# Performance work log

Hardware: AMD Instinct MI355X
Metric: run time of the kernel (lower is better)

## Reference

```python
import jax, jax.numpy as jnp
import numpy as np

B, T, N, F = 8, 24, 207, 16
H = 64            # hidden_dim
DH = 16           # dims_hyper[-1] / node-embedding out
DA = 4 * F        # temporal attention dim_out
DS = 64           # ss_gal gcn out dim (last_ss_gal_dim)
GDEP = 2
ALPHA, BETA, GAMMA = 0.05, 0.95, 0.95
TA = 2.0


def _lin(x, w, b=None):
    y = x @ w
    return y if b is None else y + b


def gcn_hyper(x, A, W, b):
    # x: [B,N,C], A: [N,N] static. h <- a*x + g * einsum('nvc,vw->nwc', h, A)
    h = x
    outs = [h]
    for _ in range(GDEP):
        h = ALPHA * x + GAMMA * jnp.einsum('bvc,vw->bwc', h, A)
        outs.append(h)
    return _lin(jnp.concatenate(outs, axis=-1), W, b)


def gcn_gru(x, A_dyn, A_sta, W, b):
    # x: [B,N,C], A_dyn: [B,N,N], A_sta: [N,N]
    h = x
    outs = [h]
    for _ in range(GDEP):
        h = (ALPHA * x
             + BETA * jnp.einsum('bvw,bvc->bwc', A_dyn, h)     # bmm(A^T, h)
             + GAMMA * jnp.einsum('bvc,vw->bwc', h, A_sta))
        outs.append(h)
    return _lin(jnp.concatenate(outs, axis=-1), W, b)


def gcn_ssgal(x, A, W, b):
    # x: [B*,N,C], A: [B*,N,N]
    h = x
    outs = [h]
    for _ in range(GDEP):
        h = ALPHA * x + GAMMA * jnp.einsum('bvw,bvc->bwc', A, h)
        outs.append(h)
    return _lin(jnp.concatenate(outs, axis=-1), W, b)


def setup_inputs() -> dict:
    key = jax.random.key(0)
    ks = jax.random.split(key, 32)
    i = iter(range(32))
    w = lambda *s: (0.02 * jax.random.normal(ks[next(i)], s, dtype=jnp.float32))
    inp = {
        'input_sequence': jax.random.normal(ks[next(i)], (B, T, N, F), dtype=jnp.float32),
        'static_adj': jax.random.uniform(ks[next(i)], (N, N), dtype=jnp.float32),
        # hyper graph generators: mlp in = (GDEP+1)*H -> DH
        'src_gen_w': w((GDEP + 1) * H, DH), 'src_gen_b': w(DH),
        'tgt_gen_w': w((GDEP + 1) * H, DH), 'tgt_gen_b': w(DH),
        # node embeddings: F -> DH
        'src_emb_w': w(F, DH), 'src_emb_b': w(DH),
        'tgt_emb_w': w(F, DH), 'tgt_emb_b': w(DH),
        # GRU gate GCNs: mlp in = (GDEP+1)*(F+H) -> H
        'gru_z_w': w((GDEP + 1) * (F + H), H), 'gru_z_b': w(H),
        'gru_r_w': w((GDEP + 1) * (F + H), H), 'gru_r_b': w(H),
        'gru_c_w': w((GDEP + 1) * (F + H), H), 'gru_c_b': w(H),
        # temporal attention: F -> DA, score DA -> 1
        'attn_q_w': w(F, DA),
        'attn_k_w': w(F, DA), 'attn_k_b': w(DA),
        'attn_s_w': w(DA, 1),
        # ss_gal spatial gcn: (GDEP+1)*F -> DS
        'sgcn_w': w((GDEP + 1) * F, DS), 'sgcn_b': w(DS),
        # predictors
        'short_w': w(DS, F), 'short_b': w(F),
        'long_w': w(H, F), 'long_b': w(F),
        'fus_w': w(DS + H, F), 'fus_b': w(F),
    }
    return inp


def _forward(input_sequence, static_adj,
             src_gen_w, src_gen_b, tgt_gen_w, tgt_gen_b,
             src_emb_w, src_emb_b, tgt_emb_w, tgt_emb_b,
             gru_z_w, gru_z_b, gru_r_w, gru_r_b, gru_c_w, gru_c_b,
             attn_q_w, attn_k_w, attn_k_b, attn_s_w,
             sgcn_w, sgcn_b,
             short_w, short_b, long_w, long_b, fus_w, fus_b):
    batch, steps, nodes = input_sequence.shape[0], input_sequence.shape[1], input_sequence.shape[2]
    eye = jnp.eye(nodes, dtype=input_sequence.dtype)

    def cell(x_t, h):
        # x_t: [B,N,F], h: [B,N,H]
        src_ctx = gcn_hyper(h, static_adj, src_gen_w, src_gen_b)   # [B,N,DH]
        tgt_ctx = gcn_hyper(h, static_adj, tgt_gen_w, tgt_gen_b)
        s = jnp.tanh(TA * _lin(x_t, src_emb_w, src_emb_b) * src_ctx)
        t = jnp.tanh(TA * _lin(x_t, tgt_emb_w, tgt_emb_b) * tgt_ctx)
        asym = jnp.einsum('bnc,bmc->bnm', s, t) - jnp.einsum('bnc,bmc->bnm', t, s)
        adj = jax.nn.relu(jnp.tanh(TA * asym)) + eye
        adj = adj / (adj.sum(axis=-1, keepdims=True) + 1e-8)
        gi = jnp.concatenate([x_t, h], axis=-1)
        z = jax.nn.sigmoid(gcn_gru(gi, adj, static_adj, gru_z_w, gru_z_b))
        r = jax.nn.sigmoid(gcn_gru(gi, adj, static_adj, gru_r_w, gru_r_b))
        ri = jnp.concatenate([x_t, r * h], axis=-1)
        c = jnp.tanh(gcn_gru(ri, adj, static_adj, gru_c_w, gru_c_b))
        return z * h + (1.0 - z) * c

    h = jnp.zeros((batch, nodes, H), dtype=input_sequence.dtype)
    for t_step in range(0, max(1, steps - 4), 4):
        h = cell(input_sequence[:, t_step], h)

    # ss_gal branch on the last 4 steps
    recent = input_sequence[:, -4:]            # [B,4,N,F]
    target = input_sequence[:, -1]             # [B,N,F]
    # temporal attention
    q = target @ attn_q_w                      # [B,N,DA]
    k = recent @ attn_k_w + attn_k_b           # [B,4,N,DA]
    scores = jnp.tanh(q[:, None, :, None, :] + k[:, :, None, :, :])  # [B,4,N,N,DA]
    scores = jnp.squeeze(scores @ attn_s_w, axis=-1)                  # [B,4,N,N]
    attn = jax.nn.softmax(scores, axis=-1)
    dyn_adj = static_adj[None] + attn.reshape(-1, nodes, nodes)       # [B*4,N,N]
    rh = recent.reshape(-1, nodes, recent.shape[-1])                  # [B*4,N,F]
    rh = gcn_ssgal(rh, dyn_adj, sgcn_w, sgcn_b)                       # [B*4,N,DS]
    rh = jax.nn.relu(rh.reshape(batch, -1, nodes, rh.shape[-1]))      # [B,4,N,DS]
    target = jnp.sum(rh, axis=1)                                       # [B,N,DS]

    short = _lin(target, short_w, short_b)      # [B,N,F]
    h = cell(short, h)                          # final GRU step on short-term prediction
    long = _lin(h, long_w, long_b)              # [B,N,F]
    fused = _lin(jnp.concatenate([target, h], axis=-1), fus_w, fus_b)  # [B,N,F]
    return jnp.stack([short, long, fused], axis=0)  # [3,B,N,F]


def reference(input_sequence, static_adj,
              src_gen_w, src_gen_b, tgt_gen_w, tgt_gen_b,
              src_emb_w, src_emb_b, tgt_emb_w, tgt_emb_b,
              gru_z_w, gru_z_b, gru_r_w, gru_r_b, gru_c_w, gru_c_b,
              attn_q_w, attn_k_w, attn_k_b, attn_s_w,
              sgcn_w, sgcn_b,
              short_w, short_b, long_w, long_b, fus_w, fus_b):
    return _forward(input_sequence, static_adj,
                    src_gen_w, src_gen_b, tgt_gen_w, tgt_gen_b,
                    src_emb_w, src_emb_b, tgt_emb_w, tgt_emb_b,
                    gru_z_w, gru_z_b, gru_r_w, gru_r_b, gru_c_w, gru_c_b,
                    attn_q_w, attn_k_w, attn_k_b, attn_s_w,
                    sgcn_w, sgcn_b,
                    short_w, short_b, long_w, long_b, fus_w, fus_b)
```

## Files before the change

kernel.cpp:

```cpp
#include <hip/hip_runtime.h>


constexpr int B = 8, T = 24, N = 207, F = 16, H = 64, DH = 16;
constexpr int PS = 208;
constexpr float ALPHA = 0.05f, BETA = 0.95f, GAMMA = 0.95f, TA = 2.0f;
constexpr int NF = N * F;
constexpr int BNF = B * N * F;

__device__ __forceinline__ float tanh_fast(float x) { float e = __expf(2.f * x); return 1.f - 2.f / (e + 1.f); }
__device__ __forceinline__ float sigm(float x) { return 1.f / (1.f + __expf(-x)); }
__device__ __forceinline__ float tanh_pnc(float x) {
    float x2 = x * x;
    float p = x * (27.f + x2);
    float q = 27.f + 9.f * x2;
    return p * __builtin_amdgcn_rcpf(q);
}

__global__ __launch_bounds__(256) void k_build_Ts(const float* __restrict__ adj, float* __restrict__ Ts) {
    int i = blockIdx.x * 256 + threadIdx.x;
    if (i >= N * N) return;
    int w = i / N, v = i % N;
    Ts[(size_t)w * PS + v] = adj[v * N + w];
}

__global__ __launch_bounds__(256) void k_mm_sq(const float* __restrict__ Ain, float* __restrict__ Aout) {
    const float* A = Ain;
    float* O = Aout;
    int w0 = blockIdx.x * 32, v0b = blockIdx.y * 32;
    int tid = threadIdx.x;
    __shared__ float sA[2][32][33], sB[2][32][33];
    float acc[4] = {0, 0, 0, 0};
    int i0 = tid >> 5, j = tid & 31;
    int r = tid >> 3, c4 = (tid & 7) * 4;
    float4 av, bv;
    auto loadT = [&](int u0) {
        av = make_float4(0, 0, 0, 0); bv = make_float4(0, 0, 0, 0);
        int w = w0 + r, u = u0 + r;
        if (w < N) av = *(const float4*)&A[(size_t)w * PS + u0 + c4];
        if (u < N) bv = *(const float4*)&A[(size_t)u * PS + v0b + c4];
    };
    loadT(0);
    int cur = 0;
    for (int t = 0; t < 7; t++) {
        __syncthreads();
        sA[cur][r][c4] = av.x; sA[cur][r][c4 + 1] = av.y; sA[cur][r][c4 + 2] = av.z; sA[cur][r][c4 + 3] = av.w;
        sB[cur][r][c4] = bv.x; sB[cur][r][c4 + 1] = bv.y; sB[cur][r][c4 + 2] = bv.z; sB[cur][r][c4 + 3] = bv.w;
        if (t < 6) loadT((t + 1) * 32);
        __syncthreads();
#pragma unroll 8
        for (int u_ = 0; u_ < 32; u_++) {
            float bvv = sB[cur][u_][j];
#pragma unroll
            for (int k = 0; k < 4; k++) acc[k] += sA[cur][i0 + k * 8][u_] * bvv;
        }
        cur ^= 1;
    }
#pragma unroll
    for (int k = 0; k < 4; k++) {
        int w = w0 + i0 + k * 8, v = v0b + j;
        if (w < N && v < N) O[(size_t)w * PS + v] = acc[k];
    }
}

__global__ __launch_bounds__(256) void k_cell_a(
    const float* __restrict__ h, const float* __restrict__ Ts, const float* __restrict__ A2,
    const float* __restrict__ xseq, int tsel, const float* __restrict__ xbuf,
    const float* __restrict__ Wsrc, const float* __restrict__ bsrc,
    const float* __restrict__ Wtgt, const float* __restrict__ btgt,
    const float* __restrict__ Wes, const float* __restrict__ bes,
    const float* __restrict__ Wet, const float* __restrict__ bet,
    float* __restrict__ s_out, float* __restrict__ t_out, float* __restrict__ catg) {
    int b = blockIdx.y, w0 = blockIdx.x * 16, lane = blockIdx.z;
    int tid = threadIdx.x, ty = tid >> 4, tx = tid & 15;
    __shared__ float sTs[2][16][33], sA2[2][16][33];
    __shared__ float sH[2][32][64];
    __shared__ float cat[16][193];
    __shared__ float sW[192][16];
    __shared__ float sX[16][16], sWe[16][16];
    float au[4] = {0, 0, 0, 0}, aw[4] = {0, 0, 0, 0};
    const float* hb = h + b * N * H;
    const float* xp = (tsel >= 0) ? (xseq + ((size_t)(b * T + tsel)) * NF) : (xbuf + (size_t)b * NF);
    int pidx = tid & 127;
    int pr = pidx >> 3, pc4 = (pidx & 7) * 4;
    float4 t4;
    float4 h4[2];
    int hr[2], hc[2];
#pragma unroll
    for (int k = 0; k < 2; k++) { int l4 = tid + k * 256; hr[k] = l4 >> 4; hc[k] = (l4 & 15) * 4; }
    auto loadT = [&](int v0) {
        t4 = make_float4(0, 0, 0, 0);
        const float* src = (tid < 128) ? Ts : A2;
        int w = w0 + pr;
        if (w < N) t4 = *(const float4*)&src[(size_t)w * PS + v0 + pc4];
#pragma unroll
        for (int k = 0; k < 2; k++) {
            float4 hv = make_float4(0, 0, 0, 0);
            int v = v0 + hr[k];
            if (v < N) hv = *(const float4*)&hb[(size_t)v * H + hc[k]];
            h4[k] = hv;
        }
    };
    loadT(0);
    int cur = 0;
    for (int t = 0; t < 7; t++) {
        __syncthreads();
        {
            float (*dst)[33] = (tid < 128) ? sTs[cur] : sA2[cur];
            dst[pr][pc4] = t4.x; dst[pr][pc4 + 1] = t4.y; dst[pr][pc4 + 2] = t4.z; dst[pr][pc4 + 3] = t4.w;
        }
#pragma unroll
        for (int k = 0; k < 2; k++) *(float4*)&sH[cur][hr[k]][hc[k]] = h4[k];
        if (t < 6) loadT((t + 1) * 32);
        __syncthreads();
#pragma unroll 8
        for (int v = 0; v < 32; v++) {
            float pu = sTs[cur][ty][v], pw = sA2[cur][ty][v];
#pragma unroll
            for (int j = 0; j < 4; j++) {
                float x = sH[cur][v][tx * 4 + j];
                au[j] += pu * x; aw[j] += pw * x;
            }
        }
        cur ^= 1;
    }
    int w = w0 + ty;
    bool valid = w < N;
    __syncthreads();
    if (valid) {
#pragma unroll
        for (int j = 0; j < 4; j++) {
            int c = tx * 4 + j;
            float hv = hb[(size_t)w * H + c];
            float u = au[j], w2 = aw[j];
            cat[ty][c] = hv;
            cat[ty][64 + c] = ALPHA * hv + GAMMA * u;
            cat[ty][128 + c] = ALPHA * hv + ALPHA * GAMMA * u + GAMMA * GAMMA * w2;
        }
    } else {
#pragma unroll
        for (int j = 0; j < 4; j++) {
            int c = tx * 4 + j;
            cat[ty][c] = 0; cat[ty][64 + c] = 0; cat[ty][128 + c] = 0;
        }
    }
    const float* Wg = lane ? Wtgt : Wsrc;
    const float* bg = lane ? btgt : bsrc;
    const float* We = lane ? Wet : Wes;
    const float* be = lane ? bet : bes;
    {
        float4 wv[3];
#pragma unroll
        for (int k = 0; k < 3; k++) wv[k] = *(const float4*)&Wg[(tid + k * 256) * 4];
        float4 xv = make_float4(0, 0, 0, 0), ev = make_float4(0, 0, 0, 0);
        int sr = 0, sc = 0;
        if (tid < 64) {
            sr = tid >> 2; sc = (tid & 3) * 4;
            int n = w0 + sr;
            if (n < N) xv = *(const float4*)&xp[(size_t)n * F + sc];
            ev = *(const float4*)&We[tid * 4];
        }
#pragma unroll
        for (int k = 0; k < 3; k++) {
            int l4 = tid + k * 256;
            int r = l4 >> 2, c4 = (l4 & 3) * 4;
            *(float4*)&sW[r][c4] = wv[k];
        }
        if (tid < 64) {
            *(float4*)&sX[sr][sc] = xv;
            *(float4*)&sWe[sr][sc] = ev;
        }
    }
    __syncthreads();
    if (lane == 0 && valid) {
#pragma unroll
        for (int j = 0; j < 5; j++) {
            int c = tx * 5 + j;
            float v = (c < 16) ? sX[ty][c] : hb[(size_t)w * H + (c - 16)];
            catg[((size_t)(b * N + w)) * 240 + c] = v;
        }
    }
    {
        float ctx = bg[tx];
#pragma unroll 8
        for (int c = 0; c < 192; c++) ctx += cat[ty][c] * sW[c][tx];
        float xe = be[tx];
#pragma unroll
        for (int f = 0; f < 16; f++) xe += sX[ty][f] * sWe[f][tx];
        if (valid) {
            float val = tanh_fast(TA * xe * ctx);
            if (lane == 0) s_out[(size_t)(b * N + w) * DH + tx] = val;
            else           t_out[(size_t)(b * N + w) * DH + tx] = val;
        }
    }
}

__global__ __launch_bounds__(256) void k_cell_bP(const float* __restrict__ s_in, const float* __restrict__ t_in,
                                                 const float* __restrict__ adj, float* __restrict__ P) {
    int b = blockIdx.y, v0 = blockIdx.x * 16;
    int tid = threadIdx.x, ty = tid >> 4, tx = tid & 15;
    __shared__ float sS[N][17], sT[N][17];
    for (int l4 = tid; l4 < 828; l4 += 256) {
        float4 sv = *(const float4*)&s_in[(size_t)b * N * 16 + l4 * 4];
        float4 tv = *(const float4*)&t_in[(size_t)b * N * 16 + l4 * 4];
        int r = l4 >> 2, c = (l4 & 3) * 4;
        sS[r][c] = sv.x; sS[r][c + 1] = sv.y; sS[r][c + 2] = sv.z; sS[r][c + 3] = sv.w;
        sT[r][c] = tv.x; sT[r][c + 1] = tv.y; sT[r][c + 2] = tv.z; sT[r][c + 3] = tv.w;
    }
    __syncthreads();
    int v = v0 + ty;
    bool valid = v < N;
    int vc = valid ? v : (N - 1);
    float sv[16], tv[16];
#pragma unroll
    for (int k = 0; k < 16; k++) { sv[k] = sS[vc][k]; tv[k] = sT[vc][k]; }
    float val[13];
    float rsum = 0.f;
#pragma unroll
    for (int idx = 0; idx < 13; idx++) {
        int w = tx + 16 * idx;
        float r = 0.f;
        if (w < N) {
            float a = 0.f;
#pragma unroll
            for (int k = 0; k < 16; k++) a += sv[k] * sT[w][k] - tv[k] * sS[w][k];
            r = tanh_fast(TA * a);
            r = r > 0.f ? r : 0.f;
            if (w == v) r += 1.f;
        }
        val[idx] = r;
        rsum += r;
    }
    float tot = rsum;
    for (int d = 8; d > 0; d >>= 1) tot += __shfl_down(tot, d, 16);
    tot = __shfl(tot, 0, 16);
    float rinv = BETA / (tot + 1e-8f);
    if (valid) {
        float* Pb = P + (size_t)b * PS * PS;
#pragma unroll
        for (int idx = 0; idx < 13; idx++) {
            int w = tx + 16 * idx;
            if (w < N) Pb[(size_t)w * PS + v] = val[idx] * rinv + GAMMA * adj[v * N + w];
        }
    }
}

__global__ __launch_bounds__(256) void k_prop1(const float* __restrict__ P, float* __restrict__ cat) {
    int b = blockIdx.y, w0 = blockIdx.x * 16, c0 = blockIdx.z * 16;
    int tid = threadIdx.x, ty = tid >> 4, tx = tid & 15;
    const float* Pb = P + (size_t)b * PS * PS;
    __shared__ float sP[2][16][33], sX[2][32][17];
    float a1 = 0.f;
    int pr = tid >> 4, pc = (tid & 15) * 2;
    int xr = tid >> 3, xc = (tid & 7) * 2;
    float2 pv, xv;
    auto loadT = [&](int v0) {
        pv = make_float2(0, 0); xv = make_float2(0, 0);
        int w = w0 + pr;
        if (w < N) pv = *(const float2*)&Pb[(size_t)w * PS + v0 + pc];
        int vv = v0 + xr;
        if (vv < N) xv = *(const float2*)&cat[((size_t)(b * N + vv)) * 240 + c0 + xc];
    };
    loadT(0);
    int cur = 0;
    for (int t = 0; t < 7; t++) {
        __syncthreads();
        sP[cur][pr][pc] = pv.x; sP[cur][pr][pc + 1] = pv.y;
        sX[cur][xr][xc] = xv.x; sX[cur][xr][xc + 1] = xv.y;
        if (t < 6) loadT((t + 1) * 32);
        __syncthreads();
#pragma unroll 8
        for (int v_ = 0; v_ < 32; v_++) a1 += sP[cur][ty][v_] * sX[cur][v_][tx];
        cur ^= 1;
    }
    int w = w0 + ty, c = c0 + tx;
    if (w < N) {
        size_t base = ((size_t)(b * N + w)) * 240;
        cat[base + 80 + c] = ALPHA * cat[base + c] + a1;
    }
}

__global__ __launch_bounds__(256) void k_gate(
    const float* __restrict__ cat, const float* __restrict__ P,
    const float* __restrict__ Wa, const float* __restrict__ ba,
    const float* __restrict__ Wb, const float* __restrict__ bb,
    int baseMode,
    const float* __restrict__ xseq, int tsel, const float* __restrict__ xbuf,
    float* __restrict__ zbuf, float* __restrict__ ricat,
    float* __restrict__ h,
    const float* __restrict__ target,
    const float* __restrict__ Wlong, const float* __restrict__ blong,
    const float* __restrict__ Wfus, const float* __restrict__ bfus,
    float* __restrict__ out) {
    int mode = baseMode + blockIdx.z;
    const float* W = (mode == 1) ? Wb : Wa;
    const float* bias = (mode == 1) ? bb : ba;
    int b = blockIdx.y, w0 = blockIdx.x * 16;
    int tid = threadIdx.x, ty = tid >> 4, tx = tid & 15;
    const float* Pb = P + (size_t)b * PS * PS;
    __shared__ float sC[16][241];
    __shared__ float sP[16][33];
    __shared__ float sX[32][81];
    __shared__ float sW[48][65];
    __shared__ float hrow[16][65], trow[16][65];
    for (int l4 = tid; l4 < 640; l4 += 256) {
        int r = l4 / 40, c4 = (l4 % 40) * 4;
        int w = w0 + r;
        float4 v4 = make_float4(0, 0, 0, 0);
        if (w < N) v4 = *(const float4*)&cat[((size_t)(b * N + w)) * 240 + c4];
        sC[r][c4] = v4.x; sC[r][c4 + 1] = v4.y; sC[r][c4 + 2] = v4.z; sC[r][c4 + 3] = v4.w;
    }
    float acc[5] = {0, 0, 0, 0, 0};
    int prr = tid >> 4, prc = (tid & 15) * 2;
    int xrow = tid & 31, xc0 = (tid >> 5) * 10;
    float2 pv;
    float2 xv[5];
    auto loadT = [&](int v0) {
        pv = make_float2(0, 0);
        int w = w0 + prr;
        if (w < N) pv = *(const float2*)&Pb[(size_t)w * PS + v0 + prc];
        int v = v0 + xrow;
#pragma unroll
        for (int k = 0; k < 5; k++) xv[k] = make_float2(0, 0);
        if (v < N) {
            const float* src = &cat[((size_t)(b * N + v)) * 240 + 80 + xc0];
#pragma unroll
            for (int k = 0; k < 5; k++) xv[k] = *(const float2*)&src[k * 2];
        }
    };
    loadT(0);
    for (int t = 0; t < 7; t++) {
        __syncthreads();
        sP[prr][prc] = pv.x; sP[prr][prc + 1] = pv.y;
#pragma unroll
        for (int k = 0; k < 5; k++) { sX[xrow][xc0 + 2 * k] = xv[k].x; sX[xrow][xc0 + 2 * k + 1] = xv[k].y; }
        if (t < 6) loadT((t + 1) * 32);
        __syncthreads();
#pragma unroll 8
        for (int v = 0; v < 32; v++) {
            float p = sP[ty][v];
#pragma unroll
            for (int j = 0; j < 5; j++) acc[j] += p * sX[v][tx * 5 + j];
        }
    }
#pragma unroll
    for (int j = 0; j < 5; j++) {
        int c = tx * 5 + j;
        sC[ty][160 + c] = ALPHA * sC[ty][c] + acc[j];
    }
    float4 wv[3];
#pragma unroll
    for (int k = 0; k < 3; k++) wv[k] = *(const float4*)&W[(tid + k * 256) * 4];
    float ga[4];
#pragma unroll
    for (int j = 0; j < 4; j++) ga[j] = bias[tx * 4 + j];
    for (int ch = 0; ch < 5; ch++) {
        __syncthreads();
#pragma unroll
        for (int k = 0; k < 3; k++) {
            int l4 = tid + k * 256;
            int r = l4 >> 4, cc = (l4 & 15) * 4;
            sW[r][cc] = wv[k].x; sW[r][cc + 1] = wv[k].y; sW[r][cc + 2] = wv[k].z; sW[r][cc + 3] = wv[k].w;
        }
        if (ch < 4) {
#pragma unroll
            for (int k = 0; k < 3; k++) wv[k] = *(const float4*)&W[(size_t)(ch + 1) * 3072 + (tid + k * 256) * 4];
        }
        __syncthreads();
        int c0 = ch * 48;
#pragma unroll 8
        for (int cc = 0; cc < 48; cc++) {
            float cv = sC[ty][c0 + cc];
#pragma unroll
            for (int j = 0; j < 4; j++) ga[j] += cv * sW[cc][tx * 4 + j];
        }
    }
    int w = w0 + ty;
    bool valid = w < N;
    if (mode == 0) {
        if (valid) {
#pragma unroll
            for (int j = 0; j < 4; j++) zbuf[((size_t)(b * N + w)) * 64 + tx * 4 + j] = sigm(ga[j]);
        }
    } else if (mode == 1) {
        if (valid) {
#pragma unroll
            for (int j = 0; j < 4; j++) {
                int o = tx * 4 + j;
                ricat[((size_t)(b * N + w)) * 240 + 16 + o] = sigm(ga[j]) * h[((size_t)(b * N + w)) * 64 + o];
            }
            if (tx < 4) {
                const float* xp = (tsel >= 0) ? (xseq + ((size_t)(b * T + tsel)) * NF) : (xbuf + (size_t)b * NF);
#pragma unroll
                for (int j = 0; j < 4; j++) {
                    int c = tx * 4 + j;
                    ricat[((size_t)(b * N + w)) * 240 + c] = xp[w * F + c];
                }
            }
        }
    } else {
#pragma unroll
        for (int j = 0; j < 4; j++) {
            int o = tx * 4 + j;
            float cval = tanh_fast(ga[j]);
            float zv = 0.f, hv = 0.f;
            if (valid) { zv = zbuf[((size_t)(b * N + w)) * 64 + o]; hv = h[((size_t)(b * N + w)) * 64 + o]; }
            float hn = zv * hv + (1.f - zv) * cval;
            if (valid) h[((size_t)(b * N + w)) * 64 + o] = hn;
            hrow[ty][o] = valid ? hn : 0.f;
        }
        if (mode == 3) {
            for (int l = tid; l < 1024; l += 256) {
                int i = l >> 6, o = l & 63;
                int ww = w0 + i;
                trow[i][o] = (ww < N) ? target[((size_t)(b * N + ww)) * 64 + o] : 0.f;
            }
            __syncthreads();
            float lg = blong[tx];
            float fs = bfus[tx];
            for (int o = 0; o < 64; o++) {
                lg += hrow[ty][o] * Wlong[o * 16 + tx];
                fs += trow[ty][o] * Wfus[o * 16 + tx] + hrow[ty][o] * Wfus[(64 + o) * 16 + tx];
            }
            if (valid) {
                out[((size_t)1 * B * N + b * N + w) * 16 + tx] = lg;
                out[((size_t)2 * B * N + b * N + w) * 16 + tx] = fs;
            }
        }
    }
}

__global__ __launch_bounds__(256) void k_attn2(const float* __restrict__ inp,
                                               const float* __restrict__ Wq, const float* __restrict__ Wk,
                                               const float* __restrict__ kb, const float* __restrict__ sw_,
                                               float* __restrict__ attnT, float* __restrict__ rsum) {
    int bt = blockIdx.z, b = bt >> 2, tau = bt & 3;
    int n0 = blockIdx.x * 32, m0 = blockIdx.y * 32;
    int tid = threadIdx.x, ti = tid >> 4, tj = tid & 15;
    __shared__ float sQ[32][65], sK[32][65];
    __shared__ float sWq[16][64], sWk[16][64];
    __shared__ float sXq[32][17], sXk[32][17];
    __shared__ float ssw[64], skb[64];
    const float* xq = inp + ((size_t)(b * T + (T - 1))) * NF;
    const float* xk = inp + ((size_t)(b * T + 20 + tau)) * NF;
    {
        float4 wq4 = *(const float4*)&Wq[tid * 4];
        float4 wk4 = *(const float4*)&Wk[tid * 4];
        *(float4*)&sWq[tid >> 4][(tid & 15) * 4] = wq4;
        *(float4*)&sWk[tid >> 4][(tid & 15) * 4] = wk4;
        if (tid < 64) { ssw[tid] = sw_[tid]; skb[tid] = kb[tid]; }
        int idx = tid & 127;
        int r = idx >> 2, c4 = (idx & 3) * 4;
        if (tid < 128) {
            float4 a = make_float4(0, 0, 0, 0);
            int n = n0 + r;
            if (n < N) a = *(const float4*)&xq[(size_t)n * F + c4];
            sXq[r][c4] = a.x; sXq[r][c4 + 1] = a.y; sXq[r][c4 + 2] = a.z; sXq[r][c4 + 3] = a.w;
        } else {
            float4 c = make_float4(0, 0, 0, 0);
            int m = m0 + r;
            if (m < N) c = *(const float4*)&xk[(size_t)m * F + c4];
            sXk[r][c4] = c.x; sXk[r][c4 + 1] = c.y; sXk[r][c4 + 2] = c.z; sXk[r][c4 + 3] = c.w;
        }
    }
    __syncthreads();
    {
        int r = tid >> 3, o0 = (tid & 7) * 8;
        float xr[16], xkr[16];
#pragma unroll
        for (int f = 0; f < 16; f++) { xr[f] = sXq[r][f]; xkr[f] = sXk[r][f]; }
#pragma unroll
        for (int j = 0; j < 8; j++) {
            int o = o0 + j;
            float aq = 0.f, ak = skb[o];
#pragma unroll
            for (int f = 0; f < 16; f++) { aq += xr[f] * sWq[f][o]; ak += xkr[f] * sWk[f][o]; }
            sQ[r][o] = aq; sK[r][o] = ak;
        }
    }
    __syncthreads();
    float s00 = 0.f, s01 = 0.f, s10 = 0.f, s11 = 0.f;
#pragma unroll 2
    for (int d = 0; d < 64; d++) {
        float w = ssw[d];
        float q1 = sQ[ti][d], q2 = sQ[ti + 16][d];
        float k1 = sK[tj][d], k2 = sK[tj + 16][d];
        s00 += tanh_pnc(q1 + k1) * w;
        s01 += tanh_pnc(q1 + k2) * w;
        s10 += tanh_pnc(q2 + k1) * w;
        s11 += tanh_pnc(q2 + k2) * w;
    }
    int n1 = n0 + ti, n2 = n0 + ti + 16, m1 = m0 + tj, m2 = m0 + tj + 16;
    bool vn1 = n1 < N, vn2 = n2 < N, vm1 = m1 < N, vm2 = m2 < N;
    float e00 = (vn1 && vm1) ? __expf(s00) : 0.f;
    float e01 = (vn1 && vm2) ? __expf(s01) : 0.f;
    float e10 = (vn2 && vm1) ? __expf(s10) : 0.f;
    float e11 = (vn2 && vm2) ? __expf(s11) : 0.f;
    float part1 = e00 + e01, part2 = e10 + e11;
    for (int d = 8; d > 0; d >>= 1) {
        part1 += __shfl_down(part1, d, 16);
        part2 += __shfl_down(part2, d, 16);
    }
    if (tj == 0) {
        if (vn1) atomicAdd(&rsum[bt * N + n1], part1);
        if (vn2) atomicAdd(&rsum[bt * N + n2], part2);
    }
    __syncthreads();
    float* tile = &sQ[0][0];
    tile[tj * 33 + ti] = e00;
    tile[(tj + 16) * 33 + ti] = e01;
    tile[tj * 33 + ti + 16] = e10;
    tile[(tj + 16) * 33 + ti + 16] = e11;
    __syncthreads();
    {
        int row = tid >> 3, c4 = (tid & 7) * 4;
        int m = m0 + row;
        if (m < N) {
            float4 v = make_float4(tile[row * 33 + c4], tile[row * 33 + c4 + 1],
                                   tile[row * 33 + c4 + 2], tile[row * 33 + c4 + 3]);
            *(float4*)&attnT[(size_t)bt * PS * PS + (size_t)m * PS + n0 + c4] = v;
        }
    }
}

__global__ __launch_bounds__(256) void k_prop_xr(const float* __restrict__ attnT, const float* __restrict__ rsum,
                                                 const float* __restrict__ Ts, const float* __restrict__ inp,
                                                 float* __restrict__ x1) {
    int bt = blockIdx.y, w0 = blockIdx.x * 16;
    int b = bt >> 2, tau = bt & 3;
    const float* xb = inp + ((size_t)(b * T + 20 + tau)) * NF;
    const float* PA = attnT + (size_t)bt * PS * PS;
    int tid = threadIdx.x, ty = tid >> 4, tx = tid & 15;
    __shared__ float sPA[2][16][33], sPT[2][16][33];
    __shared__ float sX[2][32][17], sXs[2][32][17];
    float accA = 0.f, accT = 0.f;
    int prr = tid >> 3, pcc = (tid & 7) * 4;
    int xrr = (tid - 128) >> 2, xcc = ((tid - 128) & 3) * 4;
    float4 pa, pt, xv;
    float rinv_;
    auto loadT = [&](int v0) {
        pa = make_float4(0, 0, 0, 0); pt = make_float4(0, 0, 0, 0); xv = make_float4(0, 0, 0, 0); rinv_ = 0.f;
        if (tid < 128) {
            int w = w0 + prr;
            if (w < N) {
                pa = *(const float4*)&PA[(size_t)w * PS + v0 + pcc];
                pt = *(const float4*)&Ts[(size_t)w * PS + v0 + pcc];
            }
        } else {
            int v = v0 + xrr;
            if (v < N) {
                xv = *(const float4*)&xb[(size_t)v * F + xcc];
                rinv_ = __builtin_amdgcn_rcpf(rsum[bt * N + v]);
            }
        }
    };
    loadT(0);
    int cur = 0;
    for (int t = 0; t < 7; t++) {
        __syncthreads();
        if (tid < 128) {
            sPA[cur][prr][pcc] = pa.x; sPA[cur][prr][pcc + 1] = pa.y; sPA[cur][prr][pcc + 2] = pa.z; sPA[cur][prr][pcc + 3] = pa.w;
            sPT[cur][prr][pcc] = pt.x; sPT[cur][prr][pcc + 1] = pt.y; sPT[cur][prr][pcc + 2] = pt.z; sPT[cur][prr][pcc + 3] = pt.w;
        } else {
            sX[cur][xrr][xcc] = xv.x; sX[cur][xrr][xcc + 1] = xv.y; sX[cur][xrr][xcc + 2] = xv.z; sX[cur][xrr][xcc + 3] = xv.w;
            sXs[cur][xrr][xcc] = xv.x * rinv_; sXs[cur][xrr][xcc + 1] = xv.y * rinv_;
            sXs[cur][xrr][xcc + 2] = xv.z * rinv_; sXs[cur][xrr][xcc + 3] = xv.w * rinv_;
        }
        if (t < 6) loadT((t + 1) * 32);
        __syncthreads();
#pragma unroll 8
        for (int v = 0; v < 32; v++) {
            accA += sPA[cur][ty][v] * sXs[cur][v][tx];
            accT += sPT[cur][ty][v] * sX[cur][v][tx];
// ... 135 lines not shown
                              hipStream_t stream) {
    const float* inp = (const float*)d_in[0];
    const float* adj = (const float*)d_in[1];
    const float* src_gen_w = (const float*)d_in[2];
    const float* src_gen_b = (const float*)d_in[3];
    const float* tgt_gen_w = (const float*)d_in[4];
    const float* tgt_gen_b = (const float*)d_in[5];
    const float* src_emb_w = (const float*)d_in[6];
    const float* src_emb_b = (const float*)d_in[7];
    const float* tgt_emb_w = (const float*)d_in[8];
    const float* tgt_emb_b = (const float*)d_in[9];
    const float* gru_z_w = (const float*)d_in[10];
    const float* gru_z_b = (const float*)d_in[11];
    const float* gru_r_w = (const float*)d_in[12];
    const float* gru_r_b = (const float*)d_in[13];
    const float* gru_c_w = (const float*)d_in[14];
    const float* gru_c_b = (const float*)d_in[15];
    const float* attn_q_w = (const float*)d_in[16];
    const float* attn_k_w = (const float*)d_in[17];
    const float* attn_k_b = (const float*)d_in[18];
    const float* attn_s_w = (const float*)d_in[19];
    const float* sgcn_w = (const float*)d_in[20];
    const float* sgcn_b = (const float*)d_in[21];
    const float* short_w = (const float*)d_in[22];
    const float* short_b = (const float*)d_in[23];
    const float* long_w = (const float*)d_in[24];
    const float* long_b = (const float*)d_in[25];
    const float* fus_w = (const float*)d_in[26];
    const float* fus_b = (const float*)d_in[27];
    float* out = (float*)d_out;

    float* ws = (float*)d_ws;
    size_t off = 0;
    auto A = [&](size_t n) { n = (n + 3) & ~(size_t)3; float* p = ws + off; off += n; return p; };
    float* Ts = A((size_t)PS * PS);
    float* A2 = A((size_t)PS * PS);
    float* sbuf = A((size_t)B * N * DH);
    float* tbuf = A((size_t)B * N * DH);
    float* P = A((size_t)B * PS * PS);
    float* catg = A((size_t)B * N * 240);
    float* catc = A((size_t)B * N * 240);
    float* zb = A((size_t)B * N * 64);
    float* attnT = A((size_t)32 * PS * PS);
    float* x1 = A((size_t)32 * NF);
    float* xshort = A(BNF);
    size_t zero_begin = off;
    float* h = A((size_t)B * N * H);
    float* target = A((size_t)B * N * 64);
    float* rsum = A((size_t)32 * N);
    size_t zero_end = off;
    (void)ws_size; (void)in_sizes; (void)n_in; (void)out_size;

    hipMemsetAsync(h, 0, (zero_end - zero_begin) * sizeof(float), stream);
    k_build_Ts<<<(N * N + 255) / 256, 256, 0, stream>>>(adj, Ts);
    k_mm_sq<<<dim3(7, 7), 256, 0, stream>>>(Ts, A2);

    auto run_cell = [&](int tsel, const float* xbuf, int finalFlag) {
        k_cell_a<<<dim3(13, B, 2), 256, 0, stream>>>(h, Ts, A2, inp, tsel, xbuf,
                                                     src_gen_w, src_gen_b, tgt_gen_w, tgt_gen_b,
                                                     src_emb_w, src_emb_b, tgt_emb_w, tgt_emb_b, sbuf, tbuf, catg);
        k_cell_bP<<<dim3(13, B), 256, 0, stream>>>(sbuf, tbuf, adj, P);
        k_prop1<<<dim3(13, B, 5), 256, 0, stream>>>(P, catg);
        k_gate<<<dim3(13, B, 2), 256, 0, stream>>>(catg, P, gru_z_w, gru_z_b, gru_r_w, gru_r_b, 0,
                                                   inp, tsel, xbuf, zb, catc, h,
                                                   nullptr, nullptr, nullptr, nullptr, nullptr, nullptr);
        k_prop1<<<dim3(13, B, 5), 256, 0, stream>>>(P, catc);
        k_gate<<<dim3(13, B, 1), 256, 0, stream>>>(catc, P, gru_c_w, gru_c_b, nullptr, nullptr, 2 + finalFlag,
                                                   nullptr, 0, nullptr, zb, nullptr, h,
                                                   target, long_w, long_b, fus_w, fus_b, out);
    };

    for (int t = 0; t < 20; t += 4) run_cell(t, nullptr, 0);

    k_attn2<<<dim3(7, 7, 32), 256, 0, stream>>>(inp, attn_q_w, attn_k_w, attn_k_b, attn_s_w, attnT, rsum);
    k_prop_xr<<<dim3(13, 32), 256, 0, stream>>>(attnT, rsum, Ts, inp, x1);
    k_sgc2<<<dim3(13, 32), 256, 0, stream>>>(attnT, rsum, Ts, x1, inp, sgcn_w, sgcn_b, target);
    k_short<<<dim3(13, B), 256, 0, stream>>>(target, short_w, short_b, out, xshort);

    run_cell(-1, xshort, 1);
}
```

Baseline: 645.6 us.

## Fuse first graph propagation into producers via atomic scatter; merge setup kernels

Removes both k_prop1 launches per GRU cell. The first-hop propagation is now computed as a scatter in the kernels that produce P (k_cell_bP) and the reset-gated input (k_gate mode 1), each block multiplying its P column slab by its local rows and atomically adding into the cat buffers. The buffers are pre-initialised with ALPHA*x or zero in k_cell_a. Separately, the transpose, A^2 and attention-score kernels are merged into a single k_stage0 launch, which cuts launch count but adds many global atomics and makes the float summation order nondeterministic.

New measurement: 745.5 us. +15.5%, slower.

```diff
diff --git a/kernel.cpp b/kernel.cpp
--- a/kernel.cpp
+++ b/kernel.cpp
@@ -16,49 +16,143 @@
     return p * __builtin_amdgcn_rcpf(q);
 }
 
-__global__ __launch_bounds__(256) void k_build_Ts(const float* __restrict__ adj, float* __restrict__ Ts) {
-    int i = blockIdx.x * 256 + threadIdx.x;
-    if (i >= N * N) return;
-    int w = i / N, v = i % N;
-    Ts[(size_t)w * PS + v] = adj[v * N + w];
-}
-
-__global__ __launch_bounds__(256) void k_mm_sq(const float* __restrict__ Ain, float* __restrict__ Aout) {
-    const float* A = Ain;
-    float* O = Aout;
-    int w0 = blockIdx.x * 32, v0b = blockIdx.y * 32;
-    int tid = threadIdx.x;
-    __shared__ float sA[2][32][33], sB[2][32][33];
-    float acc[4] = {0, 0, 0, 0};
-    int i0 = tid >> 5, j = tid & 31;
-    int r = tid >> 3, c4 = (tid & 7) * 4;
-    float4 av, bv;
-    auto loadT = [&](int u0) {
-        av = make_float4(0, 0, 0, 0); bv = make_float4(0, 0, 0, 0);
-        int w = w0 + r, u = u0 + r;
-        if (w < N) av = *(const float4*)&A[(size_t)w * PS + u0 + c4];
-        if (u < N) bv = *(const float4*)&A[(size_t)u * PS + v0b + c4];
-    };
-    loadT(0);
-    int cur = 0;
-    for (int t = 0; t < 7; t++) {
-        __syncthreads();
-        sA[cur][r][c4] = av.x; sA[cur][r][c4 + 1] = av.y; sA[cur][r][c4 + 2] = av.z; sA[cur][r][c4 + 3] = av.w;
-        sB[cur][r][c4] = bv.x; sB[cur][r][c4 + 1] = bv.y; sB[cur][r][c4 + 2] = bv.z; sB[cur][r][c4 + 3] = bv.w;
-        if (t < 6) loadT((t + 1) * 32);
-        __syncthreads();
-#pragma unroll 8
-        for (int u_ = 0; u_ < 32; u_++) {
-            float bvv = sB[cur][u_][j];
-#pragma unroll
-            for (int k = 0; k < 4; k++) acc[k] += sA[cur][i0 + k * 8][u_] * bvv;
-        }
-        cur ^= 1;
-    }
-#pragma unroll
-    for (int k = 0; k < 4; k++) {
-        int w = w0 + i0 + k * 8, v = v0b + j;
-        if (w < N && v < N) O[(size_t)w * PS + v] = acc[k];
+__global__ __launch_bounds__(256) void k_stage0(
+    const float* __restrict__ adj, const float* __restrict__ inp,
+    const float* __restrict__ Wq, const float* __restrict__ Wk,
+    const float* __restrict__ kb, const float* __restrict__ sw_,
+    float* __restrict__ Ts, float* __restrict__ A2,
+    float* __restrict__ attnT, float* __restrict__ rsum)
+{
+    __shared__ float smem[7424];
+    int bid = blockIdx.x, tid = threadIdx.x;
+    if (bid < 49) {
+        int vb = (bid % 7) * 32, wb = (bid / 7) * 32;
+        float* sA = smem;
+        float* sB = smem + 1056;
+        float acc[4] = {0, 0, 0, 0};
+        int i0 = tid >> 5, j = tid & 31;
+        for (int u0 = 0; u0 < N; u0 += 32) {
+            __syncthreads();
+            for (int l = tid; l < 1024; l += 256) {
+                int i = l >> 5, jj = l & 31;
+                int v = vb + i, u = u0 + jj;
+                sA[i * 33 + jj] = (v < N && u < N) ? adj[v * N + u] : 0.f;
+                int uu = u0 + i, w = wb + jj;
+                sB[i * 33 + jj] = (uu < N && w < N) ? adj[uu * N + w] : 0.f;
+            }
+            __syncthreads();
+#pragma unroll 8
+            for (int u = 0; u < 32; u++) {
+                float bv = sB[u * 33 + j];
+#pragma unroll
+                for (int k = 0; k < 4; k++) acc[k] += sA[(i0 + k * 8) * 33 + u] * bv;
+            }
+        }
+#pragma unroll
+        for (int k = 0; k < 4; k++) {
+            int v = vb + i0 + k * 8, w = wb + j;
+            if (v < N && w < N) A2[(size_t)w * PS + v] = acc[k];
+        }
+    } else if (bid < 217) {
+        int i = (bid - 49) * 256 + tid;
+        if (i < N * N) {
+            int w = i / N, v = i % N;
+            Ts[(size_t)w * PS + v] = adj[v * N + w];
+        }
+    } else {
+        int idx = bid - 217;
+        int bt = idx / 49, rem = idx % 49;
+        int n0 = (rem % 7) * 32, m0 = (rem / 7) * 32;
+        int b = bt >> 2, tau = bt & 3;
+        int ti = tid >> 4, tj = tid & 15;
+        float* sQ = smem;
+        float* sK = smem + 2080;
+        float* sWq = smem + 4160;
+        float* sWk = smem + 5184;
+        float* sXq = smem + 6208;
+        float* sXk = smem + 6752;
+        float* ssw = smem + 7296;
+        float* skb = smem + 7360;
+        const float* xq = inp + ((size_t)(b * T + (T - 1))) * NF;
+        const float* xk = inp + ((size_t)(b * T + 20 + tau)) * NF;
+        {
+            float4 wq4 = *(const float4*)&Wq[tid * 4];
+            float4 wk4 = *(const float4*)&Wk[tid * 4];
+            *(float4*)&sWq[(tid >> 4) * 64 + (tid & 15) * 4] = wq4;
+            *(float4*)&sWk[(tid >> 4) * 64 + (tid & 15) * 4] = wk4;
+            if (tid < 64) { ssw[tid] = sw_[tid]; skb[tid] = kb[tid]; }
+            int i2 = tid & 127;
+            int r = i2 >> 2, c4 = (i2 & 3) * 4;
+            if (tid < 128) {
+                float4 a = make_float4(0, 0, 0, 0);
+                int n = n0 + r;
+                if (n < N) a = *(const float4*)&xq[(size_t)n * F + c4];
+                sXq[r * 17 + c4] = a.x; sXq[r * 17 + c4 + 1] = a.y; sXq[r * 17 + c4 + 2] = a.z; sXq[r * 17 + c4 + 3] = a.w;
+            } else {
+                float4 c = make_float4(0, 0, 0, 0);
+                int m = m0 + r;
+                if (m < N) c = *(const float4*)&xk[(size_t)m * F + c4];
+                sXk[r * 17 + c4] = c.x; sXk[r * 17 + c4 + 1] = c.y; sXk[r * 17 + c4 + 2] = c.z; sXk[r * 17 + c4 + 3] = c.w;
+            }
+        }
+        __syncthreads();
+        {
+            int r = tid >> 3, o0 = (tid & 7) * 8;
+            float xr[16], xkr[16];
+#pragma unroll
+            for (int f = 0; f < 16; f++) { xr[f] = sXq[r * 17 + f]; xkr[f] = sXk[r * 17 + f]; }
+#pragma unroll
+            for (int j = 0; j < 8; j++) {
+                int o = o0 + j;
+                float aq = 0.f, ak = skb[o];
+#pragma unroll
+                for (int f = 0; f < 16; f++) { aq += xr[f] * sWq[f * 64 + o]; ak += xkr[f] * sWk[f * 64 + o]; }
+                sQ[r * 65 + o] = aq; sK[r * 65 + o] = ak;
+            }
+        }
+        __syncthreads();
+        float s00 = 0.f, s01 = 0.f, s10 = 0.f, s11 = 0.f;
+#pragma unroll 2
+        for (int d = 0; d < 64; d++) {
+            float w = ssw[d];
+            float q1 = sQ[ti * 65 + d], q2 = sQ[(ti + 16) * 65 + d];
+            float k1 = sK[tj * 65 + d], k2 = sK[(tj + 16) * 65 + d];
+            s00 += tanh_pnc(q1 + k1) * w;
+            s01 += tanh_pnc(q1 + k2) * w;
+            s10 += tanh_pnc(q2 + k1) * w;
+            s11 += tanh_pnc(q2 + k2) * w;
+        }
+        int n1 = n0 + ti, n2 = n0 + ti + 16, m1 = m0 + tj, m2 = m0 + tj + 16;
+        bool vn1 = n1 < N, vn2 = n2 < N, vm1 = m1 < N, vm2 = m2 < N;
+        float e00 = (vn1 && vm1) ? __expf(s00) : 0.f;
+        float e01 = (vn1 && vm2) ? __expf(s01) : 0.f;
+        float e10 = (vn2 && vm1) ? __expf(s10) : 0.f;
+        float e11 = (vn2 && vm2) ? __expf(s11) : 0.f;
+        float part1 = e00 + e01, part2 = e10 + e11;
+        for (int d = 8; d > 0; d >>= 1) {
+            part1 += __shfl_down(part1, d, 16);
+            part2 += __shfl_down(part2, d, 16);
+        }
+        if (tj == 0) {
+            if (vn1) atomicAdd(&rsum[bt * N + n1], part1);
+            if (vn2) atomicAdd(&rsum[bt * N + n2], part2);
+        }
+        __syncthreads();
+        float* tile = sQ;
+        tile[tj * 33 + ti] = e00;
+        tile[(tj + 16) * 33 + ti] = e01;
+        tile[tj * 33 + ti + 16] = e10;
+        tile[(tj + 16) * 33 + ti + 16] = e11;
+        __syncthreads();
+        {
+            int row = tid >> 3, c4 = (tid & 7) * 4;
+            int m = m0 + row;
+            if (m < N) {
+                float4 v = make_float4(tile[row * 33 + c4], tile[row * 33 + c4 + 1],
+                                       tile[row * 33 + c4 + 2], tile[row * 33 + c4 + 3]);
+                *(float4*)&attnT[(size_t)bt * PS * PS + (size_t)m * PS + n0 + c4] = v;
+            }
+        }
     }
 }
 
@@ -69,7 +163,8 @@
     const float* __restrict__ Wtgt, const float* __restrict__ btgt,
     const float* __restrict__ Wes, const float* __restrict__ bes,
     const float* __restrict__ Wet, const float* __restrict__ bet,
-    float* __restrict__ s_out, float* __restrict__ t_out, float* __restrict__ catg) {
+    float* __restrict__ s_out, float* __restrict__ t_out,
+    float* __restrict__ catg, float* __restrict__ catc) {
     int b = blockIdx.y, w0 = blockIdx.x * 16, lane = blockIdx.z;
     int tid = threadIdx.x, ty = tid >> 4, tx = tid & 15;
     __shared__ float sTs[2][16][33], sA2[2][16][33];
@@ -172,11 +267,14 @@
     }
     __syncthreads();
     if (lane == 0 && valid) {
+        size_t row = ((size_t)(b * N + w)) * 240;
 #pragma unroll
         for (int j = 0; j < 5; j++) {
             int c = tx * 5 + j;
             float v = (c < 16) ? sX[ty][c] : hb[(size_t)w * H + (c - 16)];
-            catg[((size_t)(b * N + w)) * 240 + c] = v;
+            catg[row + c] = v;
+            catg[row + 80 + c] = ALPHA * v;
+            catc[row + 80 + c] = 0.f;
         }
     }
     {
@@ -195,10 +293,13 @@
 }
 
 __global__ __launch_bounds__(256) void k_cell_bP(const float* __restrict__ s_in, const float* __restrict__ t_in,
-                                                 const float* __restrict__ adj, float* __restrict__ P) {
+                                                 const float* __restrict__ adj, float* __restrict__ P,
+                                                 float* __restrict__ catg) {
     int b = blockIdx.y, v0 = blockIdx.x * 16;
     int tid = threadIdx.x, ty = tid >> 4, tx = tid & 15;
     __shared__ float sS[N][17], sT[N][17];
+    __shared__ float sPcol[208][17];
+    __shared__ float sgi[16][81];
     for (int l4 = tid; l4 < 828; l4 += 256) {
         float4 sv = *(const float4*)&s_in[(size_t)b * N * 16 + l4 * 4];
         float4 tv = *(const float4*)&t_in[(size_t)b * N * 16 + l4 * 4];
@@ -206,6 +307,11 @@
         sS[r][c] = sv.x; sS[r][c + 1] = sv.y; sS[r][c + 2] = sv.z; sS[r][c + 3] = sv.w;
         sT[r][c] = tv.x; sT[r][c + 1] = tv.y; sT[r][c + 2] = tv.z; sT[r][c + 3] = tv.w;
     }
+    for (int l = tid; l < 16 * 80; l += 256) {
+        int vl = l / 80, c = l % 80;
+        int v = v0 + vl;
+        sgi[vl][c] = (v < N) ? catg[((size_t)(b * N + v)) * 240 + c] : 0.f;
+    }
     __syncthreads();
     int v = v0 + ty;
     bool valid = v < N;
@@ -234,48 +340,31 @@
     for (int d = 8; d > 0; d >>= 1) tot += __shfl_down(tot, d, 16);
     tot = __shfl(tot, 0, 16);
     float rinv = BETA / (tot + 1e-8f);
+    float* Pb = P + (size_t)b * PS * PS;
     if (valid) {
-        float* Pb = P + (size_t)b * PS * PS;
 #pragma unroll
         for (int idx = 0; idx < 13; idx++) {
             int w = tx + 16 * idx;
-            if (w < N) Pb[(size_t)w * PS + v] = val[idx] * rinv + GAMMA * adj[v * N + w];
-        }
-    }
-}
-
-__global__ __launch_bounds__(256) void k_prop1(const float* __restrict__ P, float* __restrict__ cat) {
-    int b = blockIdx.y, w0 = blockIdx.x * 16, c0 = blockIdx.z * 16;
-    int tid = threadIdx.x, ty = tid >> 4, tx = tid & 15;
-    const float* Pb = P + (size_t)b * PS * PS;
-    __shared__ float sP[2][16][33], sX[2][32][17];
-    float a1 = 0.f;
-    int pr = tid >> 4, pc = (tid & 15) * 2;
-    int xr = tid >> 3, xc = (tid & 7) * 2;
-    float2 pv, xv;
-    auto loadT = [&](int v0) {
-        pv = make_float2(0, 0); xv = make_float2(0, 0);
-        int w = w0 + pr;
-        if (w < N) pv = *(const float2*)&Pb[(size_t)w * PS + v0 + pc];
-        int vv = v0 + xr;
-        if (vv < N) xv = *(const float2*)&cat[((size_t)(b * N + vv)) * 240 + c0 + xc];
-    };
-    loadT(0);
-    int cur = 0;
-    for (int t = 0; t < 7; t++) {
-        __syncthreads();
-        sP[cur][pr][pc] = pv.x; sP[cur][pr][pc + 1] = pv.y;
-        sX[cur][xr][xc] = xv.x; sX[cur][xr][xc + 1] = xv.y;
-        if (t < 6) loadT((t + 1) * 32);
-        __syncthreads();
-#pragma unroll 8
-        for (int v_ = 0; v_ < 32; v_++) a1 += sP[cur][ty][v_] * sX[cur][v_][tx];
-        cur ^= 1;
-    }
-    int w = w0 + ty, c = c0 + tx;
-    if (w < N) {
-        size_t base = ((size_t)(b * N + w)) * 240;
-        cat[base + 80 + c] = ALPHA * cat[base + c] + a1;
+            if (w < N) {
+                float pv = val[idx] * rinv + GAMMA * adj[v * N + w];
+                Pb[(size_t)w * PS + v] = pv;
+                sPcol[w][ty] = pv;
+            }
+        }
+    } else {
+#pragma unroll
+        for (int idx = 0; idx < 13; idx++) {
+            int w = tx + 16 * idx;
+            if (w < N) sPcol[w][ty] = 0.f;
+        }
+    }
+    __syncthreads();
+    for (int o = tid; o < 207 * 80; o += 256) {
+        int w = o / 80, c = o % 80;
+        float acc = 0.f;
+#pragma unroll
+        for (int vl = 0; vl < 16; vl++) acc += sPcol[w][vl] * sgi[vl][c];
+        atomicAdd(&catg[((size_t)(b * N + w)) * 240 + 80 + c], acc);
     }
 }
 
@@ -297,17 +386,20 @@
     int b = blockIdx.y, w0 = blockIdx.x * 16;
     int tid = threadIdx.x, ty = tid >> 4, tx = tid & 15;
     const float* Pb = P + (size_t)b * PS * PS;
-    __shared__ float sC[16][241];
-    __shared__ float sP[16][33];
-    __shared__ float sX[32][81];
-    __shared__ float sW[48][65];
-    __shared__ float hrow[16][65], trow[16][65];
+    __shared__ float gsm[12176];
+    float* sC = gsm;
+    float* sP = gsm + 3856;
+    float* buf2 = gsm + 4384;
+    float* sX = buf2;
+    float* sW = buf2 + 2592;
+    float* hrow = gsm + 10096;
+    float* trow = gsm + 11136;
     for (int l4 = tid; l4 < 640; l4 += 256) {
         int r = l4 / 40, c4 = (l4 % 40) * 4;
         int w = w0 + r;
         float4 v4 = make_float4(0, 0, 0, 0);
         if (w < N) v4 = *(const float4*)&cat[((size_t)(b * N + w)) * 240 + c4];
-        sC[r][c4] = v4.x; sC[r][c4 + 1] = v4.y; sC[r][c4 + 2] = v4.z; sC[r][c4 + 3] = v4.w;
+        sC[r * 241 + c4] = v4.x; sC[r * 241 + c4 + 1] = v4.y; sC[r * 241 + c4 + 2] = v4.z; sC[r * 241 + c4 + 3] = v4.w;
     }
     float acc[5] = {0, 0, 0, 0, 0};
     int prr = tid >> 4, prc = (tid & 15) * 2;
@@ -330,22 +422,22 @@
     loadT(0);
     for (int t = 0; t < 7; t++) {
         __syncthreads();
-        sP[prr][prc] = pv.x; sP[prr][prc + 1] = pv.y;
-#pragma unroll
-        for (int k = 0; k < 5; k++) { sX[xrow][xc0 + 2 * k] = xv[k].x; sX[xrow][xc0 + 2 * k + 1] = xv[k].y; }
+        sP[prr * 33 + prc] = pv.x; sP[prr * 33 + prc + 1] = pv.y;
+#pragma unroll
+        for (int k = 0; k < 5; k++) { sX[xrow * 81 + xc0 + 2 * k] = xv[k].x; sX[xrow * 81 + xc0 + 2 * k + 1] = xv[k].y; }
         if (t < 6) loadT((t + 1) * 32);
         __syncthreads();
 #pragma unroll 8
         for (int v = 0; v < 32; v++) {
-            float p = sP[ty][v];
-#pragma unroll
-            for (int j = 0; j < 5; j++) acc[j] += p * sX[v][tx * 5 + j];
+            float p = sP[ty * 33 + v];
+#pragma unroll
+            for (int j = 0; j < 5; j++) acc[j] += p * sX[v * 81 + tx * 5 + j];
         }
     }
 #pragma unroll
     for (int j = 0; j < 5; j++) {
         int c = tx * 5 + j;
-        sC[ty][160 + c] = ALPHA * sC[ty][c] + acc[j];
+        sC[ty * 241 + 160 + c] = ALPHA * sC[ty * 241 + c] + acc[j];
     }
     float4 wv[3];
 #pragma unroll
@@ -359,7 +451,7 @@
         for (int k = 0; k < 3; k++) {
             int l4 = tid + k * 256;
             int r = l4 >> 4, cc = (l4 & 15) * 4;
-            sW[r][cc] = wv[k].x; sW[r][cc + 1] = wv[k].y; sW[r][cc + 2] = wv[k].z; sW[r][cc + 3] = wv[k].w;
+            sW[r * 65 + cc] = wv[k].x; sW[r * 65 + cc + 1] = wv[k].y; sW[r * 65 + cc + 2] = wv[k].z; sW[r * 65 + cc + 3] = wv[k].w;
         }
         if (ch < 4) {
 #pragma unroll
@@ -369,9 +461,9 @@
         int c0 = ch * 48;
 #pragma unroll 8
         for (int cc = 0; cc < 48; cc++) {
-            float cv = sC[ty][c0 + cc];
-#pragma unroll
-            for (int j = 0; j < 4; j++) ga[j] += cv * sW[cc][tx * 4 + j];
+            float cv = sC[ty * 241 + c0 + cc];
+#pragma unroll
+            for (int j = 0; j < 4; j++) ga[j] += cv * sW[cc * 65 + tx * 4 + j];
         }
     }
     int w = w0 + ty;
@@ -382,20 +474,50 @@
             for (int j = 0; j < 4; j++) zbuf[((size_t)(b * N + w)) * 64 + tx * 4 + j] = sigm(ga[j]);
         }
     } else if (mode == 1) {
+        const float* xp = (tsel >= 0) ? (xseq + ((size_t)(b * T + tsel)) * NF) : (xbuf + (size_t)b * NF);
+        float rh[4];
+#pragma unroll
+        for (int j = 0; j < 4; j++) {
+            int o = tx * 4 + j;
+            rh[j] = valid ? (sigm(ga[j]) * h[((size_t)(b * N + w)) * 64 + o]) : 0.f;
+        }
         if (valid) {
 #pragma unroll
-            for (int j = 0; j < 4; j++) {
-                int o = tx * 4 + j;
-                ricat[((size_t)(b * N + w)) * 240 + 16 + o] = sigm(ga[j]) * h[((size_t)(b * N + w)) * 64 + o];
-            }
+            for (int j = 0; j < 4; j++) ricat[((size_t)(b * N + w)) * 240 + 16 + tx * 4 + j] = rh[j];
             if (tx < 4) {
-                const float* xp = (tsel >= 0) ? (xseq + ((size_t)(b * T + tsel)) * NF) : (xbuf + (size_t)b * NF);
 #pragma unroll
                 for (int j = 0; j < 4; j++) {
                     int c = tx * 4 + j;
                     ricat[((size_t)(b * N + w)) * 240 + c] = xp[w * F + c];
                 }
             }
+        }
+        __syncthreads();
+        float* sPcol = buf2;
+        float* sri = buf2 + 3536;
+#pragma unroll
+        for (int j = 0; j < 4; j++) sri[ty * 81 + 16 + tx * 4 + j] = rh[j];
+        {
+            int vl = tid >> 4, c = tid & 15;
+            int v = w0 + vl;
+            sri[vl * 81 + c] = (v < N) ? xp[v * F + c] : 0.f;
+        }
+        for (int l4 = tid; l4 < 828; l4 += 256) {
+            int ww = l4 >> 2, q = (l4 & 3) * 4;
+            float4 p = *(const float4*)&Pb[(size_t)ww * PS + w0 + q];
+            sPcol[ww * 17 + q] = (w0 + q < N) ? p.x : 0.f;
+            sPcol[ww * 17 + q + 1] = (w0 + q + 1 < N) ? p.y : 0.f;
+            sPcol[ww * 17 + q + 2] = (w0 + q + 2 < N) ? p.z : 0.f;
+            sPcol[ww * 17 + q + 3] = (w0 + q + 3 < N) ? p.w : 0.f;
+        }
+        __syncthreads();
+        for (int o = tid; o < 207 * 80; o += 256) {
+            int ww = o / 80, c = o % 80;
+            float a2 = 0.f;
+#pragma unroll
+            for (int vl = 0; vl < 16; vl++) a2 += sPcol[ww * 17 + vl] * sri[vl * 81 + c];
+            if (ww >= w0 && ww < w0 + 16) a2 += ALPHA * sri[(ww - w0) * 81 + c];
+            atomicAdd(&ricat[((size_t)(b * N + ww)) * 240 + 80 + c], a2);
         }
     } else {
 #pragma unroll
@@ -406,118 +528,26 @@
             if (valid) { zv = zbuf[((size_t)(b * N + w)) * 64 + o]; hv = h[((size_t)(b * N + w)) * 64 + o]; }
             float hn = zv * hv + (1.f - zv) * cval;
             if (valid) h[((size_t)(b * N + w)) * 64 + o] = hn;
-            hrow[ty][o] = valid ? hn : 0.f;
+            hrow[ty * 65 + o] = valid ? hn : 0.f;
         }
         if (mode == 3) {
             for (int l = tid; l < 1024; l += 256) {
                 int i = l >> 6, o = l & 63;
                 int ww = w0 + i;
-                trow[i][o] = (ww < N) ? target[((size_t)(b * N + ww)) * 64 + o] : 0.f;
+                trow[i * 65 + o] = (ww < N) ? target[((size_t)(b * N + ww)) * 64 + o] : 0.f;
             }
             __syncthreads();
             float lg = blong[tx];
             float fs = bfus[tx];
+#pragma unroll 8
             for (int o = 0; o < 64; o++) {
-                lg += hrow[ty][o] * Wlong[o * 16 + tx];
-                fs += trow[ty][o] * Wfus[o * 16 + tx] + hrow[ty][o] * Wfus[(64 + o) * 16 + tx];
+                lg += hrow[ty * 65 + o] * Wlong[o * 16 + tx];
+                fs += trow[ty * 65 + o] * Wfus[o * 16 + tx] + hrow[ty * 65 + o] * Wfus[(64 + o) * 16 + tx];
             }
             if (valid) {
                 out[((size_t)1 * B * N + b * N + w) * 16 + tx] = lg;
                 out[((size_t)2 * B * N + b * N + w) * 16 + tx] = fs;
             }
-        }
-    }
-}
-
-__global__ __launch_bounds__(256) void k_attn2(const float* __restrict__ inp,
-                                               const float* __restrict__ Wq, const float* __restrict__ Wk,
-                                               const float* __restrict__ kb, const float* __restrict__ sw_,
-                                               float* __restrict__ attnT, float* __restrict__ rsum) {
-    int bt = blockIdx.z, b = bt >> 2, tau = bt & 3;
-    int n0 = blockIdx.x * 32, m0 = blockIdx.y * 32;
-    int tid = threadIdx.x, ti = tid >> 4, tj = tid & 15;
-    __shared__ float sQ[32][65], sK[32][65];
-    __shared__ float sWq[16][64], sWk[16][64];
-    __shared__ float sXq[32][17], sXk[32][17];
-    __shared__ float ssw[64], skb[64];
-    const float* xq = inp + ((size_t)(b * T + (T - 1))) * NF;
-    const float* xk = inp + ((size_t)(b * T + 20 + tau)) * NF;
-    {
-        float4 wq4 = *(const float4*)&Wq[tid * 4];
-        float4 wk4 = *(const float4*)&Wk[tid * 4];
-        *(float4*)&sWq[tid >> 4][(tid & 15) * 4] = wq4;
-        *(float4*)&sWk[tid >> 4][(tid & 15) * 4] = wk4;
-        if (tid < 64) { ssw[tid] = sw_[tid]; skb[tid] = kb[tid]; }
-        int idx = tid & 127;
-        int r = idx >> 2, c4 = (idx & 3) * 4;
-        if (tid < 128) {
-            float4 a = make_float4(0, 0, 0, 0);
-            int n = n0 + r;
-            if (n < N) a = *(const float4*)&xq[(size_t)n * F + c4];
-            sXq[r][c4] = a.x; sXq[r][c4 + 1] = a.y; sXq[r][c4 + 2] = a.z; sXq[r][c4 + 3] = a.w;
-        } else {
-            float4 c = make_float4(0, 0, 0, 0);
-            int m = m0 + r;
-            if (m < N) c = *(const float4*)&xk[(size_t)m * F + c4];
-            sXk[r][c4] = c.x; sXk[r][c4 + 1] = c.y; sXk[r][c4 + 2] = c.z; sXk[r][c4 + 3] = c.w;
-        }
-    }
-    __syncthreads();
-    {
-        int r = tid >> 3, o0 = (tid & 7) * 8;
-        float xr[16], xkr[16];
-#pragma unroll
-        for (int f = 0; f < 16; f++) { xr[f] = sXq[r][f]; xkr[f] = sXk[r][f]; }
-#pragma unroll
-        for (int j = 0; j < 8; j++) {
-            int o = o0 + j;
-            float aq = 0.f, ak = skb[o];
-#pragma unroll
-            for (int f = 0; f < 16; f++) { aq += xr[f] * sWq[f][o]; ak += xkr[f] * sWk[f][o]; }
-            sQ[r][o] = aq; sK[r][o] = ak;
-        }
-    }
-    __syncthreads();
-    float s00 = 0.f, s01 = 0.f, s10 = 0.f, s11 = 0.f;
-#pragma unroll 2
-    for (int d = 0; d < 64; d++) {
-        float w = ssw[d];
-        float q1 = sQ[ti][d], q2 = sQ[ti + 16][d];
-        float k1 = sK[tj][d], k2 = sK[tj + 16][d];
-        s00 += tanh_pnc(q1 + k1) * w;
-        s01 += tanh_pnc(q1 + k2) * w;
-        s10 += tanh_pnc(q2 + k1) * w;
-        s11 += tanh_pnc(q2 + k2) * w;
-    }
-    int n1 = n0 + ti, n2 = n0 + ti + 16, m1 = m0 + tj, m2 = m0 + tj + 16;
-    bool vn1 = n1 < N, vn2 = n2 < N, vm1 = m1 < N, vm2 = m2 < N;
-    float e00 = (vn1 && vm1) ? __expf(s00) : 0.f;
-    float e01 = (vn1 && vm2) ? __expf(s01) : 0.f;
-    float e10 = (vn2 && vm1) ? __expf(s10) : 0.f;
-    float e11 = (vn2 && vm2) ? __expf(s11) : 0.f;
-    float part1 = e00 + e01, part2 = e10 + e11;
-    for (int d = 8; d > 0; d >>= 1) {
-        part1 += __shfl_down(part1, d, 16);
-        part2 += __shfl_down(part2, d, 16);
-    }
-    if (tj == 0) {
-        if (vn1) atomicAdd(&rsum[bt * N + n1], part1);
-        if (vn2) atomicAdd(&rsum[bt * N + n2], part2);
-    }
-    __syncthreads();
-    float* tile = &sQ[0][0];
-    tile[tj * 33 + ti] = e00;
-    tile[(tj + 16) * 33 + ti] = e01;
-    tile[tj * 33 + ti + 16] = e10;
-    tile[(tj + 16) * 33 + ti + 16] = e11;
-    __syncthreads();
-    {
-        int row = tid >> 3, c4 = (tid & 7) * 4;
-        int m = m0 + row;
-        if (m < N) {
-            float4 v = make_float4(tile[row * 33 + c4], tile[row * 33 + c4 + 1],
-                                   tile[row * 33 + c4 + 2], tile[row * 33 + c4 + 3]);
-            *(float4*)&attnT[(size_t)bt * PS * PS + (size_t)m * PS + n0 + c4] = v;
         }
     }
 }
@@ -759,19 +789,17 @@
     (void)ws_size; (void)in_sizes; (void)n_in; (void)out_size;
 
     hipMemsetAsync(h, 0, (zero_end - zero_begin) * sizeof(float), stream);
-    k_build_Ts<<<(N * N + 255) / 256, 256, 0, stream>>>(adj, Ts);
-    k_mm_sq<<<dim3(7, 7), 256, 0, stream>>>(Ts, A2);
+    k_stage0<<<1785, 256, 0, stream>>>(adj, inp, attn_q_w, attn_k_w, attn_k_b, attn_s_w, Ts, A2, attnT, rsum);
 
     auto run_cell = [&](int tsel, const float* xbuf, int finalFlag) {
         k_cell_a<<<dim3(13, B, 2), 256, 0, stream>>>(h, Ts, A2, inp, tsel, xbuf,
                                                      src_gen_w, src_gen_b, tgt_gen_w, tgt_gen_b,
-                                                     src_emb_w, src_emb_b, tgt_emb_w, tgt_emb_b, sbuf, tbuf, catg);
-        k_cell_bP<<<dim3(13, B), 256, 0, stream>>>(sbuf, tbuf, adj, P);
-        k_prop1<<<dim3(13, B, 5), 256, 0, stream>>>(P, catg);
+                                                     src_emb_w, src_emb_b, tgt_emb_w, tgt_emb_b,
+                                                     sbuf, tbuf, catg, catc);
+        k_cell_bP<<<dim3(13, B), 256, 0, stream>>>(sbuf, tbuf, adj, P, catg);
         k_gate<<<dim3(13, B, 2), 256, 0, stream>>>(catg, P, gru_z_w, gru_z_b, gru_r_w, gru_r_b, 0,
                                                    inp, tsel, xbuf, zb, catc, h,
                                                    nullptr, nullptr, nullptr, nullptr, nullptr, nullptr);
-        k_prop1<<<dim3(13, B, 5), 256, 0, stream>>>(P, catc);
         k_gate<<<dim3(13, B, 1), 256, 0, stream>>>(catc, P, gru_c_w, gru_c_b, nullptr, nullptr, 2 + finalFlag,
                                                    nullptr, 0, nullptr, zb, nullptr, h,
                                                    target, long_w, long_b, fus_w, fus_b, out);
@@ -779,7 +807,6 @@
 
     for (int t = 0; t < 20; t += 4) run_cell(t, nullptr, 0);
 
-    k_attn2<<<dim3(7, 7, 32), 256, 0, stream>>>(inp, attn_q_w, attn_k_w, attn_k_b, attn_s_w, attnT, rsum);
     k_prop_xr<<<dim3(13, 32), 256, 0, stream>>>(attnT, rsum, Ts, inp, x1);
     k_sgc2<<<dim3(13, 32), 256, 0, stream>>>(attnT, rsum, Ts, x1, inp, sgcn_w, sgcn_b, target);
     k_short<<<dim3(13, B), 256, 0, stream>>>(target, short_w, short_b, out, xshort);
```
